# Optimization experiments

Hardware: AMD Instinct MI355X
Metric: run time of the kernel (lower is better)

## Reference

```python
import jax, jax.numpy as jnp
import numpy as np

N = 32768          # flattened tokens
D = 256            # latent_dim
K = 8192           # codebook_size
COMMIT_W = 0.25    # commitment_weight


def setup_inputs() -> dict:
    key = jax.random.key(0)
    k1, k2, k3 = jax.random.split(key, 3)
    x = jax.random.normal(k1, (N, D), dtype=jnp.float32)
    # nn.init.uniform_(embedding.weight, -1/K, 1/K)
    embedding = jax.random.uniform(k2, (K, D), dtype=jnp.float32,
                                   minval=-1.0 / K, maxval=1.0 / K)
    # out_proj: Linear(D, D, bias=False); torch default kaiming-uniform ~ U(-1/sqrt(D), 1/sqrt(D))
    lim = 1.0 / np.sqrt(D)
    w_out = jax.random.uniform(k3, (D, D), dtype=jnp.float32, minval=-lim, maxval=lim)
    return {"x": x, "embedding": embedding, "w_out": w_out}


def reference(x, embedding, w_out):
    sg = jax.lax.stop_gradient
    # codebook = out_proj(embedding.weight)  -> [K, D]
    codebook = embedding @ w_out.T
    # torch.cdist(x, codebook, p=2) is only consumed by argmin, so squared
    # Euclidean distances give the identical ids without the sqrt.
    x2 = jnp.sum(x * x, axis=1, keepdims=True)          # [N, 1]
    c2 = jnp.sum(codebook * codebook, axis=1)           # [K]
    dists = x2 - 2.0 * (x @ codebook.T) + c2            # [N, K]
    ids = jnp.argmin(dists, axis=1)                     # [N]
    q = codebook[ids]                                   # [N, D] gather
    # straight-through estimator
    quantized = x + sg(q - x)
    loss = jnp.mean((x - sg(quantized)) ** 2) \
         + COMMIT_W * jnp.mean((quantized - sg(x)) ** 2)
    return quantized, ids, loss
```

## Files before the change

kernel.cpp:

```cpp
#include <hip/hip_runtime.h>
#include <hip/hip_bf16.h>

#define N_TOK 32768
#define DIM   256
#define KCB   8192
#define CAP   64
#define MARGIN 1.75e-4f

typedef __attribute__((ext_vector_type(8))) short short8v;
typedef __attribute__((ext_vector_type(4))) float f32x4;

__device__ __forceinline__ unsigned int mono_f32(float f) {
    unsigned int u = __float_as_uint(f);
    return (u >> 31) ? ~u : (u | 0x80000000u);
}
__device__ __forceinline__ float invmono_f32(unsigned int m) {
    unsigned int u = (m & 0x80000000u) ? (m & 0x7FFFFFFFu) : ~m;
    return __uint_as_float(u);
}
__device__ __forceinline__ unsigned long long shfl_xor_u64(unsigned long long v, int m) {
    unsigned int lo = (unsigned int)v, hi = (unsigned int)(v >> 32);
    lo = __shfl_xor(lo, m, 64);
    hi = __shfl_xor(hi, m, 64);
    return ((unsigned long long)hi << 32) | lo;
}
__device__ __forceinline__ void gl_lds16(const void* g, void* l) {
    __builtin_amdgcn_global_load_lds(
        (const __attribute__((address_space(1))) unsigned int*)g,
        (__attribute__((address_space(3))) unsigned int*)l, 16, 0, 0);
}
__device__ __forceinline__ unsigned int rne16(float f) {
    unsigned int b = __float_as_uint(f);
    return (b + 0x7FFFu + ((b >> 16) & 1u)) >> 16;
}

__global__ __launch_bounds__(256) void transpose_w(const float* __restrict__ w,
                                                   float* __restrict__ wT) {
    __shared__ float tile[32][33];
    int bx = blockIdx.x & 7, by = blockIdx.x >> 3;
    int x0 = bx * 32, y0 = by * 32;
    int tx = threadIdx.x & 31, ty = threadIdx.x >> 5;
    #pragma unroll
    for (int i = 0; i < 32; i += 8)
        tile[ty + i][tx] = w[(y0 + ty + i) * DIM + x0 + tx];
    __syncthreads();
    #pragma unroll
    for (int i = 0; i < 32; i += 8)
        wT[(x0 + ty + i) * DIM + y0 + tx] = tile[tx][ty + i];
}

#define KPB 8
__global__ __launch_bounds__(256) void build_codebook(const float* __restrict__ emb,
                                                      const float* __restrict__ wT,
                                                      float* __restrict__ cb) {
    __shared__ float e[KPB][DIM];
    const int k0 = blockIdx.x * KPB;
    const int t = threadIdx.x;
    for (int i = t; i < KPB * DIM / 4; i += 256)
        ((float4*)&e[0][0])[i] = ((const float4*)(emb + (size_t)k0 * DIM))[i];
    __syncthreads();
    const int d = t;
    float acc[KPB];
    #pragma unroll
    for (int kk = 0; kk < KPB; ++kk) acc[kk] = 0.f;
    for (int j = 0; j < DIM; ++j) {
        float w = wT[j * DIM + d];
        #pragma unroll
        for (int kk = 0; kk < KPB; ++kk)
            acc[kk] = fmaf(e[kk][j], w, acc[kk]);
    }
    #pragma unroll
    for (int kk = 0; kk < KPB; ++kk)
        cb[(size_t)(k0 + kk) * DIM + d] = acc[kk];
}

__global__ __launch_bounds__(256) void sumsq_np_bf(const float* __restrict__ a,
                                                   float* __restrict__ out,
                                                   uint4* __restrict__ bfout) {
    #pragma clang fp contract(off)
    int idx = blockIdx.x * 256 + threadIdx.x;
    int r = idx >> 1, h = idx & 1;
    const float* b = a + (size_t)r * DIM + h * 128;
    uint4* dst = bfout ? bfout + ((size_t)r * 32 + h * 16) : (uint4*)0;
    float r0 = 0.f, r1 = 0.f, r2 = 0.f, r3 = 0.f,
          r4 = 0.f, r5 = 0.f, r6 = 0.f, r7 = 0.f;
    #pragma unroll
    for (int i = 0; i < 128; i += 8) {
        float4 p = *(const float4*)(b + i);
        float4 q = *(const float4*)(b + i + 4);
        if (bfout) {
            uint4 u;
            u.x = rne16(p.x) | (rne16(p.y) << 16);
            u.y = rne16(p.z) | (rne16(p.w) << 16);
            u.z = rne16(q.x) | (rne16(q.y) << 16);
            u.w = rne16(q.z) | (rne16(q.w) << 16);
            dst[i >> 3] = u;
        }
        r0 = r0 + p.x * p.x; r1 = r1 + p.y * p.y;
        r2 = r2 + p.z * p.z; r3 = r3 + p.w * p.w;
        r4 = r4 + q.x * q.x; r5 = r5 + q.y * q.y;
        r6 = r6 + q.z * q.z; r7 = r7 + q.w * q.w;
    }
    float half = ((r0 + r1) + (r2 + r3)) + ((r4 + r5) + (r6 + r7));
    float other = __shfl_xor(half, 1, 64);
    if (h == 0) out[r] = half + other;
}

__global__ __launch_bounds__(512, 2) void score_collect(
    const unsigned short* __restrict__ xbf,
    const unsigned short* __restrict__ cbbf,
    unsigned int* __restrict__ gmax,
    unsigned int* __restrict__ ccnt,
    unsigned short* __restrict__ cand)
{
    __shared__ unsigned char lds[131072];
    __shared__ float auxm[2][256];
    const int t = threadIdx.x;
    const int l = t & 63, w = t >> 6;
    const int g = l >> 4, c = l & 15;
    const int wr = w >> 1, wc = w & 1;
    const int row0 = blockIdx.x * 256;
    const int col0 = blockIdx.y * 256;

    f32x4 acc[4][8];
    #pragma unroll
    for (int m = 0; m < 4; ++m)
        #pragma unroll
        for (int n = 0; n < 8; ++n) acc[m][n] = (f32x4){0.f, 0.f, 0.f, 0.f};

    const char* xg = (const char*)xbf  + (size_t)row0 * 512;
    const char* cg = (const char*)cbbf + (size_t)col0 * 512;

#define STAGE(buf, ks)                                                         \
    do {                                                                       \
        const int kb_ = (ks) * 128;                                            \
        unsigned char* la_ = lds + (buf) * 65536;                              \
        _Pragma("unroll")                                                      \
        for (int r_ = 0; r_ < 4; ++r_) {            \
            int i_ = r_ * 512 + t;                                             \
            int row_ = i_ >> 3, pc_ = i_ & 7;                                  \
            gl_lds16(xg + (size_t)row_ * 512 + kb_ + ((pc_ ^ (row_ & 7)) * 16),\
                     la_ + i_ * 16);                                           \
        }                                                                      \
        _Pragma("unroll")                                                      \
        for (int r_ = 0; r_ < 4; ++r_) {            \
            int i_ = r_ * 512 + t;                                             \
            int row_ = i_ >> 3, pc_ = i_ & 7;                                  \
            gl_lds16(cg + (size_t)row_ * 512 + kb_ + ((pc_ ^ (row_ & 7)) * 16),\
                     la_ + 32768 + i_ * 16);                                   \
        }                                                                      \
    } while (0)

    STAGE(0, 0);
    asm volatile("s_waitcnt vmcnt(0)" ::: "memory");
    __syncthreads();

    int cur = 0;
    #pragma unroll
    for (int ks = 0; ks < 4; ++ks) {
        if (ks < 3) STAGE(cur ^ 1, ks + 1);
        const unsigned char* la = lds + cur * 65536;
        const unsigned char* lb = la + 32768;
        #pragma unroll
        for (int kk = 0; kk < 2; ++kk) {
            const int sw = ((kk * 4 + g) ^ (c & 7)) * 16;
            short8v af[4], bv[8];
            #pragma unroll
            for (int m = 0; m < 4; ++m)
                af[m] = *(const short8v*)(la + (64 * wr + 16 * m + c) * 128 + sw);
            #pragma unroll
            for (int n = 0; n < 8; ++n)
                bv[n] = *(const short8v*)(lb + (128 * wc + 16 * n + c) * 128 + sw);
            #pragma unroll
            for (int m = 0; m < 4; ++m)
                #pragma unroll
                for (int n = 0; n < 8; ++n)
                    acc[m][n] = __builtin_amdgcn_mfma_f32_16x16x32_bf16(
                        af[m], bv[n], acc[m][n], 0, 0, 0);
        }
        asm volatile("s_waitcnt vmcnt(0)" ::: "memory");
        __syncthreads();
        cur ^= 1;
    }
#undef STAGE

    #pragma unroll
    for (int m = 0; m < 4; ++m)
        #pragma unroll
        for (int j = 0; j < 4; ++j) {
            float v = acc[m][0][j];
            #pragma unroll
            for (int n = 1; n < 8; ++n) v = fmaxf(v, acc[m][n][j]);
            #pragma unroll
            for (int msk = 1; msk < 16; msk <<= 1)
                v = fmaxf(v, __shfl_xor(v, msk, 64));
            if (c == 0) auxm[wc][64 * wr + 16 * m + 4 * g + j] = v;
        }
    __syncthreads();

    if (wc == 0 && c == 0) {
        float vm[16];
        unsigned int ou[16];
        #pragma unroll
        for (int i = 0; i < 16; ++i) {
            int row = 64 * wr + 16 * (i >> 2) + 4 * g + (i & 3);
            vm[i] = fmaxf(auxm[0][row], auxm[1][row]);
        }
        #pragma unroll
        for (int i = 0; i < 16; ++i) {
            int row = 64 * wr + 16 * (i >> 2) + 4 * g + (i & 3);
            ou[i] = atomicMax(&gmax[row0 + row], mono_f32(vm[i]));
        }
        #pragma unroll
        for (int i = 0; i < 16; ++i) {
            int row = 64 * wr + 16 * (i >> 2) + 4 * g + (i & 3);
            auxm[0][row] = fmaxf(vm[i], invmono_f32(ou[i]));
        }
    }
    __syncthreads();

    #pragma unroll
    for (int m = 0; m < 4; ++m)
        #pragma unroll
        for (int j = 0; j < 4; ++j) {
            int lrow = 64 * wr + 16 * m + 4 * g + j;
            float thr = auxm[0][lrow] - MARGIN;
            #pragma unroll
            for (int n = 0; n < 8; ++n) {
                float s = acc[m][n][j];
                if (s >= thr) {
                    int row = row0 + lrow;
                    unsigned int idx = atomicAdd(&ccnt[row], 1u);
                    if (idx < CAP)
                        cand[((size_t)row << 6) + idx] =
                            (unsigned short)(col0 + 128 * wc + 16 * n + c);
                }
            }
        }
}

__device__ __forceinline__ unsigned long long np_dist_pack(
    const float4* __restrict__ xr4, const float* __restrict__ cb,
    int k, float X2, const float* __restrict__ c2)
{
    #pragma clang fp contract(off)
    const float4* cr4 = (const float4*)(cb + (size_t)k * DIM);
    float a = 0.f;
    #pragma unroll 8
    for (int t4 = 0; t4 < DIM / 4; ++t4) {
        float4 xv = xr4[t4];
        float4 cv = cr4[t4];
        a = fmaf(xv.x, cv.x, a);
        a = fmaf(xv.y, cv.y, a);
        a = fmaf(xv.z, cv.z, a);
        a = fmaf(xv.w, cv.w, a);
    }
    float u  = X2 - 2.0f * a;
    float dd = u + c2[k];
    return ((unsigned long long)mono_f32(dd) << 32) | (unsigned int)k;
}

__global__ __launch_bounds__(256) void exact_select(
    const float* __restrict__ x, const float* __restrict__ cb,
    const float* __restrict__ x2, const float* __restrict__ c2,
    const unsigned int* __restrict__ ccnt, const unsigned short* __restrict__ cand,
    unsigned long long* __restrict__ best)
{
    const int l = threadIdx.x & 63;
    const int row = (blockIdx.x * 256 + threadIdx.x) >> 6;
    const unsigned int cnt = ccnt[row];
    const float4* xr4 = (const float4*)(x + (size_t)row * DIM);
    const float X2 = x2[row];
    unsigned long long bp = ~0ull;

    if (cnt <= CAP) {
        if (l < (int)cnt) {
            int k = (int)cand[((size_t)row << 6) + l];
            bp = np_dist_pack(xr4, cb, k, X2, c2);
        }
    } else {
        for (int k = l; k < KCB; k += 64) {
            unsigned long long pk = np_dist_pack(xr4, cb, k, X2, c2);
            if (pk < bp) bp = pk;
        }
    }
    #pragma unroll
    for (int m = 1; m < 64; m <<= 1) {
        unsigned long long v = shfl_xor_u64(bp, m);
        if (v < bp) bp = v;
    }
    if (l == 0) best[row] = bp;
}

__global__ __launch_bounds__(256, 4) void score_argmin(const float* __restrict__ x,
                                                       const float* __restrict__ cb,
                                                       const float* __restrict__ c2,
                                                       const float* __restrict__ x2,
                                                       unsigned long long* __restrict__ best) {
    #pragma clang fp contract(off)
    __shared__ float As[16][128];
    __shared__ float Bs[16][128];
    const int row0 = blockIdx.x * 128;
    const int col0 = blockIdx.y * 128;
    const int t = threadIdx.x;
    const int tn = t & 15, tm = t >> 4;
    const int lrow = t >> 1, lseg = (t & 1) * 4;
    float acc[8][8];
    #pragma unroll
    for (int i = 0; i < 8; ++i)
        #pragma unroll
        for (int j = 0; j < 8; ++j) acc[i][j] = 0.f;
    const float* xp = x  + (size_t)(row0 + lrow) * DIM + lseg;
    const float* cp = cb + (size_t)(col0 + lrow) * DIM + lseg;
    for (int k0 = 0; k0 < DIM; k0 += 16) {
        float4 a0 = *(const float4*)(xp + k0);
        float4 a1 = *(const float4*)(xp + k0 + 8);
        float4 b0 = *(const float4*)(cp + k0);
        float4 b1 = *(const float4*)(cp + k0 + 8);
        __syncthreads();
        As[lseg + 0][lrow] = a0.x; As[lseg + 1][lrow] = a0.y;
        As[lseg + 2][lrow] = a0.z; As[lseg + 3][lrow] = a0.w;
        As[8 + lseg + 0][lrow] = a1.x; As[8 + lseg + 1][lrow] = a1.y;
        As[8 + lseg + 2][lrow] = a1.z; As[8 + lseg + 3][lrow] = a1.w;
        Bs[lseg + 0][lrow] = b0.x; Bs[lseg + 1][lrow] = b0.y;
        Bs[lseg + 2][lrow] = b0.z; Bs[lseg + 3][lrow] = b0.w;
        Bs[8 + lseg + 0][lrow] = b1.x; Bs[8 + lseg + 1][lrow] = b1.y;
        Bs[8 + lseg + 2][lrow] = b1.z; Bs[8 + lseg + 3][lrow] = b1.w;
        __syncthreads();
        #pragma unroll
        for (int kk = 0; kk < 16; ++kk) {
            float a[8], b[8];
            *(float4*)(a)     = *(const float4*)&As[kk][tm * 4];
            *(float4*)(a + 4) = *(const float4*)&As[kk][64 + tm * 4];
            *(float4*)(b)     = *(const float4*)&Bs[kk][tn * 4];
            *(float4*)(b + 4) = *(const float4*)&Bs[kk][64 + tn * 4];
            #pragma unroll
            for (int i = 0; i < 8; ++i)
                #pragma unroll
                for (int j = 0; j < 8; ++j)
                    acc[i][j] = fmaf(a[i], b[j], acc[i][j]);
        }
    }
    float c2v[8], x2v[8];
    #pragma unroll
    for (int j = 0; j < 4; ++j) {
        c2v[j]     = c2[col0 + tn * 4 + j];
        c2v[4 + j] = c2[col0 + 64 + tn * 4 + j];
    }
    #pragma unroll
    for (int i = 0; i < 4; ++i) {
        x2v[i]     = x2[row0 + tm * 4 + i];
        x2v[4 + i] = x2[row0 + 64 + tm * 4 + i];
    }
    #pragma unroll
    for (int i = 0; i < 8; ++i) {
        unsigned long long bp = ~0ull;
        #pragma unroll
        for (int j = 0; j < 8; ++j) {
            float tt = 2.0f * acc[i][j];
            float u  = x2v[i] - tt;
            float dd = u + c2v[j];
            int id = col0 + ((j < 4) ? (tn * 4 + j) : (64 + tn * 4 + (j - 4)));
            unsigned long long pk = ((unsigned long long)mono_f32(dd) << 32) | (unsigned int)id;
            if (pk < bp) bp = pk;
        }
        #pragma unroll
        for (int m = 1; m < 16; m <<= 1) {
            unsigned long long v = shfl_xor_u64(bp, m);
            if (v < bp) bp = v;
        }
        if (tn == 0) {
            int gr = row0 + ((i < 4) ? (tm * 4 + i) : (64 + tm * 4 + (i - 4)));
            atomicMin(&best[gr], bp);
        }
    }
}

__global__ __launch_bounds__(256) void finalize(const float* __restrict__ x,
                                                const float* __restrict__ cb,
                                                const unsigned long long* __restrict__ best,
                                                float* __restrict__ out,
                                                float* __restrict__ partial) {
    const int r = blockIdx.x;
    const int d = threadIdx.x;
    const int id = (int)(best[r] & 0xFFFFFFFFu);
    const float q  = cb[(size_t)id * DIM + d];
    const float xv = x[(size_t)r * DIM + d];
    out[(size_t)r * DIM + d] = q;
    float df = xv - q;
    float v = df * df;
    #pragma unroll
    for (int o = 32; o > 0; o >>= 1) v += __shfl_down(v, o, 64);
    __shared__ float w4[4];
    if ((d & 63) == 0) w4[d >> 6] = v;
    __syncthreads();
    if (d == 0) {
        partial[r] = w4[0] + w4[1] + w4[2] + w4[3];
        out[(size_t)N_TOK * DIM + r] = (float)id;
    }
}

__global__ __launch_bounds__(256) void reduce_loss(const float* __restrict__ partial,
                                                   float* __restrict__ out) {
    float s = 0.f;
    for (int i = threadIdx.x; i < N_TOK / 4; i += 256) {
        float4 v = ((const float4*)partial)[i];
        s += (v.x + v.y) + (v.z + v.w);
    }
    #pragma unroll
    for (int o = 32; o > 0; o >>= 1) s += __shfl_down(s, o, 64);
    __shared__ float w4[4];
    if ((threadIdx.x & 63) == 0) w4[threadIdx.x >> 6] = s;
    __syncthreads();
    if (threadIdx.x == 0)
        out[(size_t)N_TOK * DIM + N_TOK] =
            (w4[0] + w4[1] + w4[2] + w4[3]) * (1.25f / ((float)N_TOK * (float)DIM));
}

extern "C" void kernel_launch(void* const* d_in, const int* in_sizes, int n_in,
                              void* d_out, int out_size, void* d_ws, size_t ws_size,
                              hipStream_t stream) {
    const float* x     = (const float*)d_in[0];
    const float* emb   = (const float*)d_in[1];
    const float* w_out = (const float*)d_in[2];
    float* out = (float*)d_out;

    char* ws = (char*)d_ws;
    unsigned long long* best = (unsigned long long*)ws;
    float* x2 = (float*)(ws + 262400);
    float* wT = (float*)(ws + 393472);
    float* cb = (float*)(ws + 655616);
    float* c2 = (float*)(ws + 9044224);
    unsigned int*   gmax = (unsigned int*)(ws + 9076992);
    unsigned int*   ccnt = (unsigned int*)(ws + 9208064);
    unsigned short* cand = (unsigned short*)(ws + 9339136);
    unsigned short* xbf  = (unsigned short*)(ws + 13533440);
    unsigned short* cbbf = (unsigned short*)(ws + 30310656);
    float* partial = wT;
    const size_t NEED = 34504960;
    const bool useMfma = (ws_size >= NEED);

    transpose_w   <<<64,  256, 0, stream>>>(w_out, wT);
    build_codebook<<<KCB / KPB, 256, 0, stream>>>(emb, wT, cb);
    sumsq_np_bf   <<<N_TOK * 2 / 256, 256, 0, stream>>>(x, x2,
                      useMfma ? (uint4*)xbf : (uint4*)0);
    sumsq_np_bf   <<<KCB * 2 / 256, 256, 0, stream>>>(cb, c2,
                      useMfma ? (uint4*)cbbf : (uint4*)0);

    if (useMfma) {
        hipMemsetAsync(gmax, 0, 262144, stream);
        score_collect <<<dim3(N_TOK / 256, KCB / 256), 512, 0, stream>>>(
            xbf, cbbf, gmax, ccnt, cand);
        exact_select  <<<N_TOK / 4, 256, 0, stream>>>(x, cb, x2, c2, ccnt, cand, best);
    } else {
        hipMemsetAsync(best, 0xFF, 262144, stream);
        score_argmin  <<<dim3(N_TOK / 128, KCB / 128), 256, 0, stream>>>(x, cb, c2, x2, best);
    }

    finalize      <<<N_TOK, 256, 0, stream>>>(x, cb, best, out, partial);
    reduce_loss   <<<1, 256, 0, stream>>>(partial, out);
}
```

Baseline: 525.1 us.

## Swizzle score grid, deepen GEMM prefetch, and vectorize finalize per block

The score_collect grid becomes 1D with a grouped block-index swizzle, so blocks that run together share codebook tiles in cache. Its K loop is unrolled with two stages in flight, using partial vmcnt waits and raw s_barrier instead of a full wait plus __syncthreads each step. finalize now handles 16 rows per block with float4 loads and writes one partial per block, so reduce_loss sums 2048 values instead of 32768. The partial vmcnt counts must match the number of loads issued per stage, or the LDS data could be read before it has arrived.

```diff
diff --git a/kernel.cpp b/kernel.cpp
--- a/kernel.cpp
+++ b/kernel.cpp
@@ -119,8 +119,11 @@
     const int l = t & 63, w = t >> 6;
     const int g = l >> 4, c = l & 15;
     const int wr = w >> 1, wc = w & 1;
-    const int row0 = blockIdx.x * 256;
-    const int col0 = blockIdx.y * 256;
+    const int bid = blockIdx.x;
+    const int bx = (bid & 7) + 8 * ((bid >> 3) & 15);
+    const int by = bid >> 7;
+    const int row0 = bx * 256;
+    const int col0 = by * 256;
 
     f32x4 acc[4][8];
     #pragma unroll
@@ -151,38 +154,58 @@
         }                                                                      \
     } while (0)
 
-    STAGE(0, 0);
+#define COMPUTE(buf)                                                           \
+    do {                                                                       \
+        const unsigned char* la_ = lds + (buf) * 65536;                        \
+        const unsigned char* lb_ = la_ + 32768;                                \
+        _Pragma("unroll")                                                      \
+        for (int kk = 0; kk < 2; ++kk) {                                       \
+            const int sw_ = ((kk * 4 + g) ^ (c & 7)) * 16;                     \
+            short8v af[4], bv[8];                                              \
+            _Pragma("unroll")                                                  \
+            for (int m = 0; m < 4; ++m)                                        \
+                af[m] = *(const short8v*)(la_ + (64 * wr + 16 * m + c) * 128 + sw_); \
+            _Pragma("unroll")                                                  \
+            for (int n = 0; n < 8; ++n)                                        \
+                bv[n] = *(const short8v*)(lb_ + (128 * wc + 16 * n + c) * 128 + sw_); \
+            _Pragma("unroll")                                                  \
+            for (int m = 0; m < 4; ++m)                                        \
+                _Pragma("unroll")                                              \
+                for (int n = 0; n < 8; ++n)                                    \
+                    acc[m][n] = __builtin_amdgcn_mfma_f32_16x16x32_bf16(       \
+                        af[m], bv[n], acc[m][n], 0, 0, 0);                     \
+        }                                                                      \
+    } while (0)
+
+    STAGE(0, 0); STAGE(1, 1);
+    asm volatile("s_waitcnt vmcnt(8)" ::: "memory");
+    __builtin_amdgcn_s_barrier();
+    asm volatile("" ::: "memory");
+
+    COMPUTE(0);
+    __builtin_amdgcn_s_barrier();
+    asm volatile("" ::: "memory");
+    STAGE(0, 2);
+    asm volatile("s_waitcnt vmcnt(8)" ::: "memory");
+    __builtin_amdgcn_s_barrier();
+    asm volatile("" ::: "memory");
+
+    COMPUTE(1);
+    __builtin_amdgcn_s_barrier();
+    asm volatile("" ::: "memory");
+    STAGE(1, 3);
+    asm volatile("s_waitcnt vmcnt(8)" ::: "memory");
+    __builtin_amdgcn_s_barrier();
+    asm volatile("" ::: "memory");
+
+    COMPUTE(0);
     asm volatile("s_waitcnt vmcnt(0)" ::: "memory");
-    __syncthreads();
-
-    int cur = 0;
-    #pragma unroll
-    for (int ks = 0; ks < 4; ++ks) {
-        if (ks < 3) STAGE(cur ^ 1, ks + 1);
-        const unsigned char* la = lds + cur * 65536;
-        const unsigned char* lb = la + 32768;
-        #pragma unroll
-        for (int kk = 0; kk < 2; ++kk) {
-            const int sw = ((kk * 4 + g) ^ (c & 7)) * 16;
-            short8v af[4], bv[8];
-            #pragma unroll
-            for (int m = 0; m < 4; ++m)
-                af[m] = *(const short8v*)(la + (64 * wr + 16 * m + c) * 128 + sw);
-            #pragma unroll
-            for (int n = 0; n < 8; ++n)
-                bv[n] = *(const short8v*)(lb + (128 * wc + 16 * n + c) * 128 + sw);
-            #pragma unroll
-            for (int m = 0; m < 4; ++m)
-                #pragma unroll
-                for (int n = 0; n < 8; ++n)
-                    acc[m][n] = __builtin_amdgcn_mfma_f32_16x16x32_bf16(
-                        af[m], bv[n], acc[m][n], 0, 0, 0);
-        }
-        asm volatile("s_waitcnt vmcnt(0)" ::: "memory");
-        __syncthreads();
-        cur ^= 1;
-    }
+    __builtin_amdgcn_s_barrier();
+    asm volatile("" ::: "memory");
+
+    COMPUTE(1);
 #undef STAGE
+#undef COMPUTE
 
     #pragma unroll
     for (int m = 0; m < 4; ++m)
@@ -381,29 +404,42 @@
                                                 const unsigned long long* __restrict__ best,
                                                 float* __restrict__ out,
                                                 float* __restrict__ partial) {
-    const int r = blockIdx.x;
-    const int d = threadIdx.x;
+    __shared__ float rsum[16];
+    const int t = threadIdx.x;
+    const int rloc = t >> 4, seg = t & 15;
+    const int r = blockIdx.x * 16 + rloc;
     const int id = (int)(best[r] & 0xFFFFFFFFu);
-    const float q  = cb[(size_t)id * DIM + d];
-    const float xv = x[(size_t)r * DIM + d];
-    out[(size_t)r * DIM + d] = q;
-    float df = xv - q;
-    float v = df * df;
-    #pragma unroll
-    for (int o = 32; o > 0; o >>= 1) v += __shfl_down(v, o, 64);
-    __shared__ float w4[4];
-    if ((d & 63) == 0) w4[d >> 6] = v;
-    __syncthreads();
-    if (d == 0) {
-        partial[r] = w4[0] + w4[1] + w4[2] + w4[3];
+    const float4* xp = (const float4*)(x  + (size_t)r  * DIM) + seg * 4;
+    const float4* cp = (const float4*)(cb + (size_t)id * DIM) + seg * 4;
+    float4*       op = (float4*)(out + (size_t)r * DIM) + seg * 4;
+    float s = 0.f;
+    #pragma unroll
+    for (int i = 0; i < 4; ++i) {
+        float4 xv = xp[i], qv = cp[i];
+        op[i] = qv;
+        float dx = xv.x - qv.x, dy = xv.y - qv.y;
+        float dz = xv.z - qv.z, dw = xv.w - qv.w;
+        s += dx * dx + dy * dy + dz * dz + dw * dw;
+    }
+    #pragma unroll
+    for (int m = 1; m < 16; m <<= 1) s += __shfl_xor(s, m, 64);
+    if (seg == 0) {
+        rsum[rloc] = s;
         out[(size_t)N_TOK * DIM + r] = (float)id;
+    }
+    __syncthreads();
+    if (t == 0) {
+        float bs = 0.f;
+        #pragma unroll
+        for (int i = 0; i < 16; ++i) bs += rsum[i];
+        partial[blockIdx.x] = bs;
     }
 }
 
 __global__ __launch_bounds__(256) void reduce_loss(const float* __restrict__ partial,
                                                    float* __restrict__ out) {
     float s = 0.f;
-    for (int i = threadIdx.x; i < N_TOK / 4; i += 256) {
+    for (int i = threadIdx.x; i < 2048 / 4; i += 256) {
         float4 v = ((const float4*)partial)[i];
         s += (v.x + v.y) + (v.z + v.w);
     }
@@ -449,14 +485,13 @@
 
     if (useMfma) {
         hipMemsetAsync(gmax, 0, 262144, stream);
-        score_collect <<<dim3(N_TOK / 256, KCB / 256), 512, 0, stream>>>(
-            xbf, cbbf, gmax, ccnt, cand);
+        score_collect <<<4096, 512, 0, stream>>>(xbf, cbbf, gmax, ccnt, cand);
         exact_select  <<<N_TOK / 4, 256, 0, stream>>>(x, cb, x2, c2, ccnt, cand, best);
     } else {
         hipMemsetAsync(best, 0xFF, 262144, stream);
         score_argmin  <<<dim3(N_TOK / 128, KCB / 128), 256, 0, stream>>>(x, cb, c2, x2, best);
     }
 
-    finalize      <<<N_TOK, 256, 0, stream>>>(x, cb, best, out, partial);
+    finalize      <<<N_TOK / 16, 256, 0, stream>>>(x, cb, best, out, partial);
     reduce_loss   <<<1, 256, 0, stream>>>(partial, out);
 }
```

New measurement: 514.7 us. 1.02x faster.
